# Performance work log

Hardware: AMD Instinct MI355X
Metric: run time of the kernel (lower is better)

The kernel has to match this reference:

```python
import jax, jax.numpy as jnp
import numpy as np

NEG = -1e30  # safe -inf surrogate (avoids nan grads through where)
NUM_CLASSES = 128
BLANK = NUM_CLASSES - 1
B, T, L = 256, 512, 64


def setup_inputs() -> dict:
    key = jax.random.key(0)
    k1, k2, k3, k4 = jax.random.split(key, 4)
    y_pred = jax.random.normal(k1, (B, T, NUM_CLASSES), dtype=jnp.float32)
    y_true = jax.random.randint(k2, (B, L), 0, BLANK, dtype=jnp.int32)  # labels in [0, C-2]
    input_length = jax.random.randint(k3, (B,), T // 2, T + 1, dtype=jnp.int32)
    label_length = jax.random.randint(k4, (B,), L // 2, L + 1, dtype=jnp.int32)
    return {"y_true": y_true, "y_pred": y_pred,
            "input_length": input_length, "label_length": label_length}


def ctc_loss(y_pred, y_true, input_length, label_length):
    # y_pred: [B,T,C] logits (batch-major), y_true: [B,L] int labels, blank = C-1.
    Bs, Ts, C = y_pred.shape
    Ls = y_true.shape[1]
    S = 2 * Ls + 1  # extended label lattice: blank, l1, blank, l2, ..., blank
    lp = jax.nn.log_softmax(y_pred.astype(jnp.float32), axis=-1)  # [B,T,C]
    z = jnp.full((Bs, S), BLANK, dtype=jnp.int32).at[:, 1::2].set(y_true)  # [B,S]
    idx = jnp.broadcast_to(z[:, None, :], (Bs, Ts, S))
    lp_z = jnp.take_along_axis(lp, idx, axis=2)  # [B,T,S] log p(z_s | t)
    # skip transition s-2 -> s allowed when z_s is a label differing from z_{s-2}
    s_idx = jnp.arange(S)
    z_m2 = jnp.pad(z[:, :-2], ((0, 0), (2, 0)), constant_values=BLANK)
    skip = (s_idx[None, :] >= 2) & (z != BLANK) & (z != z_m2)  # [B,S]
    alpha0 = (jnp.full((Bs, S), NEG, jnp.float32)
              .at[:, 0].set(lp_z[:, 0, 0])
              .at[:, 1].set(lp_z[:, 0, 1]))
    lps = jnp.moveaxis(lp_z[:, 1:, :], 1, 0)  # [T-1, B, S]
    ts = jnp.arange(1, Ts)

    def step(alpha, xs):
        t, lpt = xs
        a1 = jnp.pad(alpha[:, :-1], ((0, 0), (1, 0)), constant_values=NEG)
        a2 = jnp.where(skip, jnp.pad(alpha[:, :-2], ((0, 0), (2, 0)), constant_values=NEG), NEG)
        new = jnp.logaddexp(jnp.logaddexp(alpha, a1), a2) + lpt
        # freeze rows whose sequence already ended (t >= input_length)
        alpha = jnp.where((t < input_length)[:, None], new, alpha)
        return alpha, None

    alphaT, _ = jax.lax.scan(step, alpha0, (ts, lps))
    e1 = (2 * label_length)[:, None]  # final blank position per row
    a_end = jnp.take_along_axis(alphaT, e1, axis=1)[:, 0]
    a_end2 = jnp.take_along_axis(alphaT, e1 - 1, axis=1)[:, 0]
    return -jnp.logaddexp(a_end, a_end2)  # [B] negative log-likelihood


def reference(y_true, y_pred, input_length, label_length):
    # tf.nn.ctc_loss(labels, logits, label_length, logit_length,
    #                logits_time_major=False, blank_index=num_classes-1)
    return ctc_loss(y_pred, y_true, input_length, label_length)
```

## Files before the change

### kernel.cpp

```cpp
#include <hip/hip_runtime.h>
#include <hip/hip_fp16.h>
#include <math.h>


constexpr int Cc = 128;
constexpr int Tt = 512;
constexpr int Ll = 64;
constexpr float INV_LN2 = 1.4426950408889634f;
constexpr float LN2_F   = 0.6931471805599453f;

__device__ __forceinline__ float fexp2(float x) { return __builtin_amdgcn_exp2f(x); }
__device__ __forceinline__ float flog2(float x) { return __builtin_amdgcn_logf(x); }

template<int CTRL, bool BC>
__device__ __forceinline__ float dppf(float old, float x) {
    return __int_as_float(__builtin_amdgcn_update_dpp(
        __float_as_int(old), __float_as_int(x), CTRL, 0xF, 0xF, BC));
}
__device__ __forceinline__ float wshr1(float x, float fill) { return dppf<0x138, false>(fill, x); }

__device__ __forceinline__ float rlf(float v, int lane) {
    return __int_as_float(__builtin_amdgcn_readlane(__float_as_int(v), lane));
}

__device__ __forceinline__ float rowsum(float e) {
    e += dppf<0x111, true>(0.f, e);
    e += dppf<0x112, true>(0.f, e);
    e += dppf<0x114, true>(0.f, e);
    e += dppf<0x118, true>(0.f, e);
    return e;
}
__device__ __forceinline__ float rowmax(float m) {
    m = fmaxf(m, dppf<0x111, true>(0.f, m));
    m = fmaxf(m, dppf<0x112, true>(0.f, m));
    m = fmaxf(m, dppf<0x114, true>(0.f, m));
    m = fmaxf(m, dppf<0x118, true>(0.f, m));
    return m;
}
__device__ __forceinline__ float allsum(float e) {
    e = rowsum(e);
    return (rlf(e, 15) + rlf(e, 31)) + (rlf(e, 47) + rlf(e, 63));
}
__device__ __forceinline__ float allmax(float m) {
    m = rowmax(m);
    return fmaxf(fmaxf(rlf(m, 15), rlf(m, 31)), fmaxf(rlf(m, 47), rlf(m, 63)));
}

__device__ __forceinline__ float bperm_f(int srclane, float v) {
    return __int_as_float(__builtin_amdgcn_ds_bpermute(srclane << 2, __float_as_int(v)));
}
__device__ __forceinline__ float gather4(float4 v, int srclane, int csel) {
    const float gx = bperm_f(srclane, v.x), gy = bperm_f(srclane, v.y);
    const float gz = bperm_f(srclane, v.z), gw = bperm_f(srclane, v.w);
    const float lo = (csel & 1) ? gy : gx;
    const float hi = (csel & 1) ? gw : gz;
    return (csel & 2) ? hi : lo;
}

__global__ __launch_bounds__(256, 1) void ctc_fused_kernel(
    const int* __restrict__ y_true,
    const float* __restrict__ y_pred,
    const int* __restrict__ in_len,
    const int* __restrict__ lab_len,
    float* __restrict__ lpb_ws,
    float* __restrict__ out)
{
    __shared__ __half w_lds[Tt * 64];

    const int b   = blockIdx.x;
    const int tid = threadIdx.x;
    const int w   = tid >> 6;
    const int l   = tid & 63;

    const int lab = y_true[b * Ll + l] & 127;
    const float* rowbase = y_pred + (size_t)b * Tt * Cc;
    float* lpb = lpb_ws + b * Tt;

    const int half = l >> 5, li = l & 31;
    const int srcA = lab >> 2;
    const int csel = lab & 3;
    const int tbase = w * 128;

    float4 vb[4];
#pragma unroll
    for (int j = 0; j < 4; ++j)
        vb[j] = ((const float4*)(rowbase + (size_t)(tbase + 2 * j + half) * Cc))[li];

    for (int i = 0; i < 64; i += 4) {
#pragma unroll
        for (int j = 0; j < 4; ++j) {
            const float4 v = vb[j];
            const int nx = i + 4 + j;
            if (nx < 64)
                vb[j] = ((const float4*)(rowbase + (size_t)(tbase + 2 * nx + half) * Cc))[li];

            const int rA = tbase + 2 * (i + j);
            const int rB = rA + 1;

            float e = (fexp2(v.x * INV_LN2) + fexp2(v.y * INV_LN2))
                    + (fexp2(v.z * INV_LN2) + fexp2(v.w * INV_LN2));
            e = rowsum(e);
            const float sA = rlf(e, 15) + rlf(e, 31);
            const float sB = rlf(e, 47) + rlf(e, 63);
            const float lsA = flog2(sA), lsB = flog2(sB);

            const float blA = rlf(v.w, 31);
            const float blB = rlf(v.w, 63);

            if (l == 0) {
                lpb[rA] = fmaf(blA, INV_LN2, -lsA);
                lpb[rB] = fmaf(blB, INV_LN2, -lsB);
            }

            const float xA = gather4(v, srcA, csel);
            const float xB = gather4(v, srcA + 32, csel);
            const float wA = fminf(fmaxf(fexp2((xA - blA) * INV_LN2), 6.1e-5f), 8192.0f);
            const float wB = fminf(fmaxf(fexp2((xB - blB) * INV_LN2), 6.1e-5f), 8192.0f);
            w_lds[rA * 64 + l] = __float2half(wA);
            w_lds[rB * 64 + l] = __float2half(wB);
        }
    }

    __syncthreads();
    if (w != 0) return;

    const int inlen = in_len[b];
    const int LLv   = lab_len[b];

    const int labp  = __shfl_up(lab, 1, 64);
    const float skf = ((l >= 1) && (lab != labp)) ? 1.0f : 0.0f;

    float cb8[8];
#pragma unroll
    for (int j = 0; j < 8; ++j) cb8[j] = lpb[j * 64 + l];

    float aO = 0.0f, aE = 0.0f, r0 = 1.0f;
    float Rtot = 0.0f;

#define STEP(W) {                                                         \
        const float pE = wshr1(aE, r0);      \
        const float pO = wshr1(aO, 0.0f);                 \
        const float nO = (fmaf(skf, pO, pE) + aO) * (W);                  \
        aE += aO;                                                         \
        aO = nO; }

#define RENORM() {                                                        \
        const float M_ = allmax(fmaxf(fmaxf(aO, aE), r0));                \
        int R_ = (int)(__float_as_uint(M_) >> 23) - 127;                  \
        R_ = (R_ < 0) ? 0 : ((R_ > 126) ? 126 : R_);                      \
        const float sc = __uint_as_float((unsigned)(127 - R_) << 23);     \
        aO = fminf(aO * sc, 4.0f);                                        \
        aE = fminf(aE * sc, 4.0f);                                        \
        r0 = fminf(r0 * sc, 4.0f);                                        \
        Rtot += (float)R_; }

    __half hA[8], hB[8];
#pragma unroll
    for (int q = 0; q < 8; ++q) hA[q] = w_lds[q * 64 + l];

    const int nfull = inlen >> 3;
    for (int cb = 0; cb < nfull; ++cb) {
        const int nx = (cb + 1 < Tt / 8) ? cb + 1 : Tt / 8 - 1;
#pragma unroll
        for (int q = 0; q < 8; ++q) hB[q] = w_lds[(nx * 8 + q) * 64 + l];
#pragma unroll
        for (int j = 0; j < 8; ++j) STEP(__half2float(hA[j]));
        RENORM();
#pragma unroll
        for (int q = 0; q < 8; ++q) hA[q] = hB[q];
    }
    const int t0 = nfull << 3;
    if (t0 < inlen) {
#pragma unroll
        for (int j = 0; j < 8; ++j)
            if (t0 + j < inlen) STEP(__half2float(hA[j]));
    }
#undef STEP
#undef RENORM

    float s = 0.0f;
#pragma unroll
    for (int j = 0; j < 8; ++j) s += (j * 64 + l < inlen) ? cb8[j] : 0.0f;
    const float cum_b = allsum(s);

    const float aEr = __shfl(aE, LLv - 1, 64);
    const float aOr = __shfl(aO, LLv - 1, 64);
    if (l == 0)
        out[b] = -LN2_F * (flog2(fmaxf(aEr + aOr, 1e-37f)) + Rtot + cum_b);
}

extern "C" void kernel_launch(void* const* d_in, const int* in_sizes, int n_in,
                              void* d_out, int out_size, void* d_ws, size_t ws_size,
                              hipStream_t stream) {
    const int*   y_true  = (const int*)d_in[0];
    const float* y_pred  = (const float*)d_in[1];
    const int*   in_len  = (const int*)d_in[2];
    const int*   lab_len = (const int*)d_in[3];
    float*       out     = (float*)d_out;
    float*       lpb_ws  = (float*)d_ws;

    ctc_fused_kernel<<<256, 256, 0, stream>>>(y_true, y_pred, in_len, lab_len, lpb_ws, out);
}
```

Baseline: 128.9 us.

## Split CTC into prep and chain kernels with packed fp16 weights in global workspace

Splits the fused kernel into a prep kernel that computes log-softmax blank terms and fp16 emission weights and writes them to a global workspace, packed as eight timesteps per lane in a uint4. A separate one-wave-per-batch chain kernel then runs the recursion, reading 128-bit loads prefetched 64 timesteps ahead. The aim is to take the LDS staging and the 3-of-4-idle-wave recursion out of the prep block and to make the weight loads wide. In exchange it adds a second launch and a round trip of the weights through global memory. A fused fallback is kept for small workspaces, and weights for lanes past the label length are zeroed.

Result: slower. 143.3 us (+11.2%).

```diff
diff --git a/kernel.cpp b/kernel.cpp
--- a/kernel.cpp
+++ b/kernel.cpp
@@ -6,6 +6,7 @@
 constexpr int Cc = 128;
 constexpr int Tt = 512;
 constexpr int Ll = 64;
+constexpr int NC = Tt / 8;
 constexpr float INV_LN2 = 1.4426950408889634f;
 constexpr float LN2_F   = 0.6931471805599453f;
 
@@ -22,7 +23,6 @@
 __device__ __forceinline__ float rlf(float v, int lane) {
     return __int_as_float(__builtin_amdgcn_readlane(__float_as_int(v), lane));
 }
-
 __device__ __forceinline__ float rowsum(float e) {
     e += dppf<0x111, true>(0.f, e);
     e += dppf<0x112, true>(0.f, e);
@@ -45,7 +45,6 @@
     m = rowmax(m);
     return fmaxf(fmaxf(rlf(m, 15), rlf(m, 31)), fmaxf(rlf(m, 47), rlf(m, 63)));
 }
-
 __device__ __forceinline__ float bperm_f(int srclane, float v) {
     return __int_as_float(__builtin_amdgcn_ds_bpermute(srclane << 2, __float_as_int(v)));
 }
@@ -57,29 +56,27 @@
     return (csel & 2) ? hi : lo;
 }
 
-__global__ __launch_bounds__(256, 1) void ctc_fused_kernel(
-    const int* __restrict__ y_true,
-    const float* __restrict__ y_pred,
-    const int* __restrict__ in_len,
+__global__ __launch_bounds__(256, 1) void ctc_prep_kernel(
+    const int* __restrict__ y_true, const float* __restrict__ y_pred,
     const int* __restrict__ lab_len,
-    float* __restrict__ lpb_ws,
-    float* __restrict__ out)
+    float* __restrict__ lpb_ws, __half* __restrict__ w_ws)
 {
-    __shared__ __half w_lds[Tt * 64];
-
     const int b   = blockIdx.x;
     const int tid = threadIdx.x;
     const int w   = tid >> 6;
     const int l   = tid & 63;
 
+    int LLv = lab_len[b]; if (LLv < 1) LLv = 1; if (LLv > Ll) LLv = Ll;
     const int lab = y_true[b * Ll + l] & 127;
     const float* rowbase = y_pred + (size_t)b * Tt * Cc;
     float* lpb = lpb_ws + b * Tt;
+    __half* wbase = w_ws + ((size_t)b * NC) * 64 * 8;
 
     const int half = l >> 5, li = l & 31;
     const int srcA = lab >> 2;
     const int csel = lab & 3;
     const int tbase = w * 128;
+    const bool live = (l < LLv);
 
     float4 vb[4];
 #pragma unroll
@@ -87,6 +84,7 @@
         vb[j] = ((const float4*)(rowbase + (size_t)(tbase + 2 * j + half) * Cc))[li];
 
     for (int i = 0; i < 64; i += 4) {
+        unsigned pw[4];
 #pragma unroll
         for (int j = 0; j < 4; ++j) {
             const float4 v = vb[j];
@@ -103,80 +101,223 @@
             const float sA = rlf(e, 15) + rlf(e, 31);
             const float sB = rlf(e, 47) + rlf(e, 63);
             const float lsA = flog2(sA), lsB = flog2(sB);
-
             const float blA = rlf(v.w, 31);
             const float blB = rlf(v.w, 63);
 
-            if (l == 0) {
-                lpb[rA] = fmaf(blA, INV_LN2, -lsA);
-                lpb[rB] = fmaf(blB, INV_LN2, -lsB);
-            }
+            if (l == 0)
+                ((float2*)(lpb + rA))[0] =
+                    make_float2(fmaf(blA, INV_LN2, -lsA), fmaf(blB, INV_LN2, -lsB));
 
             const float xA = gather4(v, srcA, csel);
             const float xB = gather4(v, srcA + 32, csel);
-            const float wA = fminf(fmaxf(fexp2((xA - blA) * INV_LN2), 6.1e-5f), 8192.0f);
-            const float wB = fminf(fmaxf(fexp2((xB - blB) * INV_LN2), 6.1e-5f), 8192.0f);
-            w_lds[rA * 64 + l] = __float2half(wA);
-            w_lds[rB * 64 + l] = __float2half(wB);
+            float wA = fminf(fmaxf(fexp2((xA - blA) * INV_LN2), 6.1e-5f), 8192.0f);
+            float wB = fminf(fmaxf(fexp2((xB - blB) * INV_LN2), 6.1e-5f), 8192.0f);
+            wA = live ? wA : 0.0f;
+            wB = live ? wB : 0.0f;
+            pw[j] = (unsigned)__half_as_ushort(__float2half(wA))
+                  | ((unsigned)__half_as_ushort(__float2half(wB)) << 16);
+        }
+        const int chunk = (tbase + 2 * i) >> 3;
+        ((uint4*)(wbase + ((size_t)chunk * 64 + l) * 8))[0] =
+            make_uint4(pw[0], pw[1], pw[2], pw[3]);
+    }
+}
+
+template<bool GUARD>
+__device__ __forceinline__ void do_chunk(uint4 raw, int t0, int inlen, float skf,
+                                         float& aO, float& aE, float& r0, float& Rtot)
+{
+    float dv[8];
+    {
+        const __half2 h0 = *reinterpret_cast<const __half2*>(&raw.x);
+        const __half2 h1 = *reinterpret_cast<const __half2*>(&raw.y);
+        const __half2 h2 = *reinterpret_cast<const __half2*>(&raw.z);
+        const __half2 h3 = *reinterpret_cast<const __half2*>(&raw.w);
+        dv[0] = __low2float(h0); dv[1] = __high2float(h0);
+        dv[2] = __low2float(h1); dv[3] = __high2float(h1);
+        dv[4] = __low2float(h2); dv[5] = __high2float(h2);
+        dv[6] = __low2float(h3); dv[7] = __high2float(h3);
+    }
+#pragma unroll
+    for (int j = 0; j < 8; ++j) {
+        if (!GUARD || (t0 + j < inlen)) {
+            const float pE = wshr1(aE, r0);
+            const float pO = wshr1(aO, 0.0f);
+            const float nO = (fmaf(skf, pO, pE) + aO) * dv[j];
+            aE += aO;
+            aO = nO;
+        }
+    }
+    const float M_ = allmax(fmaxf(fmaxf(aO, aE), r0));
+    int R_ = (int)(__float_as_uint(M_) >> 23) - 127;
+    R_ = (R_ < 0) ? 0 : ((R_ > 126) ? 126 : R_);
+    const float sc = __uint_as_float((unsigned)(127 - R_) << 23);
+    aO = fminf(aO * sc, 4.0f);
+    aE = fminf(aE * sc, 4.0f);
+    r0 = fminf(r0 * sc, 4.0f);
+    Rtot += (float)R_;
+}
+
+__global__ __launch_bounds__(64, 1) void ctc_chain_kernel(
+    const int* __restrict__ y_true, const int* __restrict__ in_len,
+    const int* __restrict__ lab_len,
+    const float* __restrict__ lpb_ws, const __half* __restrict__ w_ws,
+    float* __restrict__ out)
+{
+    const int b = blockIdx.x;
+    const int l = threadIdx.x;
+
+    int inlen = in_len[b]; if (inlen < 1) inlen = 1; if (inlen > Tt) inlen = Tt;
+    int LLv   = lab_len[b]; if (LLv < 1) LLv = 1; if (LLv > Ll) LLv = Ll;
+
+    const int lab  = y_true[b * Ll + l] & 127;
+    const int labp = __shfl_up(lab, 1, 64);
+    const float skf = ((l >= 1) && (lab != labp)) ? 1.0f : 0.0f;
+
+    const float* lpb = lpb_ws + b * Tt;
+    const uint4* wp  = (const uint4*)w_ws + (size_t)b * NC * 64;
+
+    float cb8[8];
+#pragma unroll
+    for (int j = 0; j < 8; ++j) cb8[j] = lpb[j * 64 + l];
+
+#define LOADGRP(G, BUF) { _Pragma("unroll")                               \
+        for (int c = 0; c < 8; ++c) BUF[c] = wp[(size_t)(((G) * 8 + c) * 64 + l)]; }
+
+    float aO = 0.0f, aE = 0.0f, r0 = 1.0f, Rtot = 0.0f;
+
+    uint4 A[8], Bv[8];
+    LOADGRP(0, A);
+
+    for (int g = 0; ; ) {
+        const int base = g * 64;
+        const bool full = (base + 64 <= inlen);
+        const bool last = (base + 64 >= inlen);
+        if (!last) LOADGRP(g + 1, Bv);
+        if (full) {
+#pragma unroll
+            for (int c = 0; c < 8; ++c)
+                do_chunk<false>(A[c], base + 8 * c, inlen, skf, aO, aE, r0, Rtot);
+        } else {
+#pragma unroll
+            for (int c = 0; c < 8; ++c) {
+                const int t0 = base + 8 * c;
+                if (t0 < inlen)
+                    do_chunk<true>(A[c], t0, inlen, skf, aO, aE, r0, Rtot);
+            }
+        }
+        if (last) break;
+#pragma unroll
+        for (int c = 0; c < 8; ++c) A[c] = Bv[c];
+        ++g;
+    }
+#undef LOADGRP
+
+    float s = 0.0f;
+#pragma unroll
+    for (int j = 0; j < 8; ++j) s += (j * 64 + l < inlen) ? cb8[j] : 0.0f;
+    const float cum_b = allsum(s);
+
+    const float aEr = __shfl(aE, LLv - 1, 64);
+    const float aOr = __shfl(aO, LLv - 1, 64);
+    if (l == 0)
+        out[b] = -LN2_F * (flog2(fmaxf(aEr + aOr, 1e-37f)) + Rtot + cum_b);
+}
+
+__global__ __launch_bounds__(256, 1) void ctc_fused_kernel(
+    const int* __restrict__ y_true, const float* __restrict__ y_pred,
+    const int* __restrict__ in_len, const int* __restrict__ lab_len,
+    float* __restrict__ lpb_ws, float* __restrict__ out)
+{
+    __shared__ __half w_lds[Tt * 64];
+
+    const int b   = blockIdx.x;
+    const int tid = threadIdx.x;
+    const int w   = tid >> 6;
+    const int l   = tid & 63;
+
+    int LLv = lab_len[b]; if (LLv < 1) LLv = 1; if (LLv > Ll) LLv = Ll;
+    const int lab = y_true[b * Ll + l] & 127;
+    const float* rowbase = y_pred + (size_t)b * Tt * Cc;
+    float* lpb = lpb_ws + b * Tt;
+
+    const int half = l >> 5, li = l & 31;
+    const int srcA = lab >> 2, csel = lab & 3;
+    const int tbase = w * 128;
+    const bool live = (l < LLv);
+
+    float4 vb[4];
+#pragma unroll
+    for (int j = 0; j < 4; ++j)
+        vb[j] = ((const float4*)(rowbase + (size_t)(tbase + 2 * j + half) * Cc))[li];
+
+    for (int i = 0; i < 64; i += 4) {
+#pragma unroll
+        for (int j = 0; j < 4; ++j) {
+            const float4 v = vb[j];
+            const int nx = i + 4 + j;
+            if (nx < 64)
+                vb[j] = ((const float4*)(rowbase + (size_t)(tbase + 2 * nx + half) * Cc))[li];
+            const int rA = tbase + 2 * (i + j), rB = rA + 1;
+            float e = (fexp2(v.x * INV_LN2) + fexp2(v.y * INV_LN2))
+                    + (fexp2(v.z * INV_LN2) + fexp2(v.w * INV_LN2));
+            e = rowsum(e);
+            const float sA = rlf(e, 15) + rlf(e, 31);
+            const float sB = rlf(e, 47) + rlf(e, 63);
+            const float lsA = flog2(sA), lsB = flog2(sB);
+            const float blA = rlf(v.w, 31), blB = rlf(v.w, 63);
+            if (l == 0)
+                ((float2*)(lpb + rA))[0] =
+                    make_float2(fmaf(blA, INV_LN2, -lsA), fmaf(blB, INV_LN2, -lsB));
+            const float xA = gather4(v, srcA, csel);
+            const float xB = gather4(v, srcA + 32, csel);
+            float wA = fminf(fmaxf(fexp2((xA - blA) * INV_LN2), 6.1e-5f), 8192.0f);
+            float wB = fminf(fmaxf(fexp2((xB - blB) * INV_LN2), 6.1e-5f), 8192.0f);
+            w_lds[rA * 64 + l] = __float2half(live ? wA : 0.0f);
+            w_lds[rB * 64 + l] = __float2half(live ? wB : 0.0f);
         }
     }
 
     __syncthreads();
     if (w != 0) return;
 
-    const int inlen = in_len[b];
-    const int LLv   = lab_len[b];
-
-    const int labp  = __shfl_up(lab, 1, 64);
+    int inlen = in_len[b]; if (inlen < 1) inlen = 1; if (inlen > Tt) inlen = Tt;
+    const int labp = __shfl_up(lab, 1, 64);
     const float skf = ((l >= 1) && (lab != labp)) ? 1.0f : 0.0f;
 
     float cb8[8];
 #pragma unroll
     for (int j = 0; j < 8; ++j) cb8[j] = lpb[j * 64 + l];
 
-    float aO = 0.0f, aE = 0.0f, r0 = 1.0f;
-    float Rtot = 0.0f;
-
-#define STEP(W) {                                                         \
-        const float pE = wshr1(aE, r0);      \
-        const float pO = wshr1(aO, 0.0f);                 \
-        const float nO = (fmaf(skf, pO, pE) + aO) * (W);                  \
-        aE += aO;                                                         \
-        aO = nO; }
-
-#define RENORM() {                                                        \
-        const float M_ = allmax(fmaxf(fmaxf(aO, aE), r0));                \
-        int R_ = (int)(__float_as_uint(M_) >> 23) - 127;                  \
-        R_ = (R_ < 0) ? 0 : ((R_ > 126) ? 126 : R_);                      \
-        const float sc = __uint_as_float((unsigned)(127 - R_) << 23);     \
-        aO = fminf(aO * sc, 4.0f);                                        \
-        aE = fminf(aE * sc, 4.0f);                                        \
-        r0 = fminf(r0 * sc, 4.0f);                                        \
-        Rtot += (float)R_; }
-
-    __half hA[8], hB[8];
-#pragma unroll
-    for (int q = 0; q < 8; ++q) hA[q] = w_lds[q * 64 + l];
+    float aO = 0.0f, aE = 0.0f, r0 = 1.0f, Rtot = 0.0f;
 
     const int nfull = inlen >> 3;
     for (int cb = 0; cb < nfull; ++cb) {
-        const int nx = (cb + 1 < Tt / 8) ? cb + 1 : Tt / 8 - 1;
-#pragma unroll
-        for (int q = 0; q < 8; ++q) hB[q] = w_lds[(nx * 8 + q) * 64 + l];
-#pragma unroll
-        for (int j = 0; j < 8; ++j) STEP(__half2float(hA[j]));
-        RENORM();
-#pragma unroll
-        for (int q = 0; q < 8; ++q) hA[q] = hB[q];
+        uint4 raw;
+        raw.x = *(const unsigned*)&w_lds[(cb * 8 + 0) * 64 + l * 2 / 2];
+        unsigned p0 = ((unsigned)__half_as_ushort(w_lds[(cb * 8 + 0) * 64 + l]))
+                    | ((unsigned)__half_as_ushort(w_lds[(cb * 8 + 1) * 64 + l]) << 16);
+        unsigned p1 = ((unsigned)__half_as_ushort(w_lds[(cb * 8 + 2) * 64 + l]))
+                    | ((unsigned)__half_as_ushort(w_lds[(cb * 8 + 3) * 64 + l]) << 16);
+        unsigned p2 = ((unsigned)__half_as_ushort(w_lds[(cb * 8 + 4) * 64 + l]))
+                    | ((unsigned)__half_as_ushort(w_lds[(cb * 8 + 5) * 64 + l]) << 16);
+        unsigned p3 = ((unsigned)__half_as_ushort(w_lds[(cb * 8 + 6) * 64 + l]))
+                    | ((unsigned)__half_as_ushort(w_lds[(cb * 8 + 7) * 64 + l]) << 16);
+        raw = make_uint4(p0, p1, p2, p3);
+        do_chunk<false>(raw, cb * 8, inlen, skf, aO, aE, r0, Rtot);
     }
     const int t0 = nfull << 3;
     if (t0 < inlen) {
-#pragma unroll
-        for (int j = 0; j < 8; ++j)
-            if (t0 + j < inlen) STEP(__half2float(hA[j]));
-    }
-#undef STEP
-#undef RENORM
+        unsigned p[4] = {0, 0, 0, 0};
+#pragma unroll
+        for (int j = 0; j < 8; ++j) {
+            if (t0 + j < Tt) {
+                const unsigned hv = __half_as_ushort(w_lds[(t0 + j) * 64 + l]);
+                p[j >> 1] |= hv << ((j & 1) * 16);
+            }
+        }
+        do_chunk<true>(make_uint4(p[0], p[1], p[2], p[3]), t0, inlen, skf, aO, aE, r0, Rtot);
+    }
 
     float s = 0.0f;
 #pragma unroll
@@ -197,7 +338,16 @@
     const int*   in_len  = (const int*)d_in[2];
     const int*   lab_len = (const int*)d_in[3];
     float*       out     = (float*)d_out;
-    float*       lpb_ws  = (float*)d_ws;
-
-    ctc_fused_kernel<<<256, 256, 0, stream>>>(y_true, y_pred, in_len, lab_len, lpb_ws, out);
-}
+
+    const size_t lpb_bytes = (size_t)256 * Tt * sizeof(float);
+    const size_t w_bytes   = (size_t)256 * NC * 64 * 8 * sizeof(__half);
+    float*  lpb = (float*)d_ws;
+    __half* wws = (__half*)((char*)d_ws + lpb_bytes);
+
+    if (ws_size >= lpb_bytes + w_bytes) {
+        ctc_prep_kernel<<<256, 256, 0, stream>>>(y_true, y_pred, lab_len, lpb, wws);
+        ctc_chain_kernel<<<256, 64, 0, stream>>>(y_true, in_len, lab_len, lpb, wws, out);
+    } else {
+        ctc_fused_kernel<<<256, 256, 0, stream>>>(y_true, y_pred, in_len, lab_len, lpb, out);
+    }
+}
```

## Widen preprocessing to 16 waves, pack fp16 weights per lane, drop workspace

Applied to the files above, without the earlier changes.

The block grows from 4 to 16 waves, so the log-softmax and weight preprocessing phase is split over four times as many threads and each wave handles 32 timesteps. The blank log-prob sum is now reduced in registers and shared memory rather than written to a global workspace and read back. The LDS weight layout becomes [chunk][lane][8], so the recurrence wave fetches 8 timesteps with one 16-byte load, and the tail chunk is handled by a guarded template. Weights for labels past label_length are zeroed, and the serial recurrence is still done by a single wave.

New measurement: 117.4 us. 8.9% less time.

```diff
diff --git a/kernel.cpp b/kernel.cpp
--- a/kernel.cpp
+++ b/kernel.cpp
@@ -22,7 +22,6 @@
 __device__ __forceinline__ float rlf(float v, int lane) {
     return __int_as_float(__builtin_amdgcn_readlane(__float_as_int(v), lane));
 }
-
 __device__ __forceinline__ float rowsum(float e) {
     e += dppf<0x111, true>(0.f, e);
     e += dppf<0x112, true>(0.f, e);
@@ -37,15 +36,10 @@
     m = fmaxf(m, dppf<0x118, true>(0.f, m));
     return m;
 }
-__device__ __forceinline__ float allsum(float e) {
-    e = rowsum(e);
-    return (rlf(e, 15) + rlf(e, 31)) + (rlf(e, 47) + rlf(e, 63));
-}
 __device__ __forceinline__ float allmax(float m) {
     m = rowmax(m);
     return fmaxf(fmaxf(rlf(m, 15), rlf(m, 31)), fmaxf(rlf(m, 47), rlf(m, 63)));
 }
-
 __device__ __forceinline__ float bperm_f(int srclane, float v) {
     return __int_as_float(__builtin_amdgcn_ds_bpermute(srclane << 2, __float_as_int(v)));
 }
@@ -57,41 +51,81 @@
     return (csel & 2) ? hi : lo;
 }
 
-__global__ __launch_bounds__(256, 1) void ctc_fused_kernel(
+template<bool GUARD>
+__device__ __forceinline__ void do_chunk(uint4 raw, int t0, int inlen, float skf,
+                                         float& aO, float& aE, float& r0, float& Rtot)
+{
+    float dv[8];
+    {
+        const __half2 h0 = *reinterpret_cast<const __half2*>(&raw.x);
+        const __half2 h1 = *reinterpret_cast<const __half2*>(&raw.y);
+        const __half2 h2 = *reinterpret_cast<const __half2*>(&raw.z);
+        const __half2 h3 = *reinterpret_cast<const __half2*>(&raw.w);
+        dv[0] = __low2float(h0); dv[1] = __high2float(h0);
+        dv[2] = __low2float(h1); dv[3] = __high2float(h1);
+        dv[4] = __low2float(h2); dv[5] = __high2float(h2);
+        dv[6] = __low2float(h3); dv[7] = __high2float(h3);
+    }
+#pragma unroll
+    for (int j = 0; j < 8; ++j) {
+        if (!GUARD || (t0 + j < inlen)) {
+            const float pE = wshr1(aE, r0);
+            const float pO = wshr1(aO, 0.0f);
+            const float nO = (fmaf(skf, pO, pE) + aO) * dv[j];
+            aE += aO;
+            aO = nO;
+        }
+    }
+    const float M_ = allmax(fmaxf(fmaxf(aO, aE), r0));
+    int R_ = (int)(__float_as_uint(M_) >> 23) - 127;
+    R_ = (R_ < 0) ? 0 : ((R_ > 126) ? 126 : R_);
+    const float sc = __uint_as_float((unsigned)(127 - R_) << 23);
+    aO = fminf(aO * sc, 4.0f);
+    aE = fminf(aE * sc, 4.0f);
+    r0 = fminf(r0 * sc, 4.0f);
+    Rtot += (float)R_;
+}
+
+__global__ __launch_bounds__(1024, 1) void ctc_fused2_kernel(
     const int* __restrict__ y_true,
     const float* __restrict__ y_pred,
     const int* __restrict__ in_len,
     const int* __restrict__ lab_len,
-    float* __restrict__ lpb_ws,
     float* __restrict__ out)
 {
-    __shared__ __half w_lds[Tt * 64];
+    __shared__ __half w_lds[Tt / 8][64][8];
+    __shared__ float  ps[16];
 
     const int b   = blockIdx.x;
     const int tid = threadIdx.x;
     const int w   = tid >> 6;
     const int l   = tid & 63;
 
+    int inlen = in_len[b]; if (inlen < 1) inlen = 1; if (inlen > Tt) inlen = Tt;
+    int LLv   = lab_len[b]; if (LLv < 1) LLv = 1; if (LLv > Ll) LLv = Ll;
+
     const int lab = y_true[b * Ll + l] & 127;
     const float* rowbase = y_pred + (size_t)b * Tt * Cc;
-    float* lpb = lpb_ws + b * Tt;
 
     const int half = l >> 5, li = l & 31;
     const int srcA = lab >> 2;
     const int csel = lab & 3;
-    const int tbase = w * 128;
+    const int tbase = w * 32;
+    const bool live = (l < LLv);
 
     float4 vb[4];
 #pragma unroll
     for (int j = 0; j < 4; ++j)
         vb[j] = ((const float4*)(rowbase + (size_t)(tbase + 2 * j + half) * Cc))[li];
 
-    for (int i = 0; i < 64; i += 4) {
+    float acc = 0.0f;
+
+    for (int i = 0; i < 16; i += 4) {
 #pragma unroll
         for (int j = 0; j < 4; ++j) {
             const float4 v = vb[j];
             const int nx = i + 4 + j;
-            if (nx < 64)
+            if (nx < 16)
                 vb[j] = ((const float4*)(rowbase + (size_t)(tbase + 2 * nx + half) * Cc))[li];
 
             const int rA = tbase + 2 * (i + j);
@@ -103,85 +137,49 @@
             const float sA = rlf(e, 15) + rlf(e, 31);
             const float sB = rlf(e, 47) + rlf(e, 63);
             const float lsA = flog2(sA), lsB = flog2(sB);
-
             const float blA = rlf(v.w, 31);
             const float blB = rlf(v.w, 63);
 
-            if (l == 0) {
-                lpb[rA] = fmaf(blA, INV_LN2, -lsA);
-                lpb[rB] = fmaf(blB, INV_LN2, -lsB);
-            }
+            const float lpbA = fmaf(blA, INV_LN2, -lsA);
+            const float lpbB = fmaf(blB, INV_LN2, -lsB);
+            acc += ((rA < inlen) ? lpbA : 0.0f) + ((rB < inlen) ? lpbB : 0.0f);
 
             const float xA = gather4(v, srcA, csel);
             const float xB = gather4(v, srcA + 32, csel);
-            const float wA = fminf(fmaxf(fexp2((xA - blA) * INV_LN2), 6.1e-5f), 8192.0f);
-            const float wB = fminf(fmaxf(fexp2((xB - blB) * INV_LN2), 6.1e-5f), 8192.0f);
-            w_lds[rA * 64 + l] = __float2half(wA);
-            w_lds[rB * 64 + l] = __float2half(wB);
+            float wA = fminf(fmaxf(fexp2((xA - blA) * INV_LN2), 6.1e-5f), 8192.0f);
+            float wB = fminf(fmaxf(fexp2((xB - blB) * INV_LN2), 6.1e-5f), 8192.0f);
+            wA = live ? wA : 0.0f;
+            wB = live ? wB : 0.0f;
+            const unsigned packed =
+                  (unsigned)__half_as_ushort(__float2half(wA))
+                | ((unsigned)__half_as_ushort(__float2half(wB)) << 16);
+            *(unsigned*)&w_lds[rA >> 3][l][rA & 7] = packed;
         }
     }
+    if (l == 0) ps[w] = acc;
 
     __syncthreads();
     if (w != 0) return;
 
-    const int inlen = in_len[b];
-    const int LLv   = lab_len[b];
-
-    const int labp  = __shfl_up(lab, 1, 64);
+    const int labp = __shfl_up(lab, 1, 64);
     const float skf = ((l >= 1) && (lab != labp)) ? 1.0f : 0.0f;
 
-    float cb8[8];
-#pragma unroll
-    for (int j = 0; j < 8; ++j) cb8[j] = lpb[j * 64 + l];
-
-    float aO = 0.0f, aE = 0.0f, r0 = 1.0f;
-    float Rtot = 0.0f;
-
-#define STEP(W) {                                                         \
-        const float pE = wshr1(aE, r0);      \
-        const float pO = wshr1(aO, 0.0f);                 \
-        const float nO = (fmaf(skf, pO, pE) + aO) * (W);                  \
-        aE += aO;                                                         \
-        aO = nO; }
-
-#define RENORM() {                                                        \
-        const float M_ = allmax(fmaxf(fmaxf(aO, aE), r0));                \
-        int R_ = (int)(__float_as_uint(M_) >> 23) - 127;                  \
-        R_ = (R_ < 0) ? 0 : ((R_ > 126) ? 126 : R_);                      \
-        const float sc = __uint_as_float((unsigned)(127 - R_) << 23);     \
-        aO = fminf(aO * sc, 4.0f);                                        \
-        aE = fminf(aE * sc, 4.0f);                                        \
-        r0 = fminf(r0 * sc, 4.0f);                                        \
-        Rtot += (float)R_; }
-
-    __half hA[8], hB[8];
-#pragma unroll
-    for (int q = 0; q < 8; ++q) hA[q] = w_lds[q * 64 + l];
-
-    const int nfull = inlen >> 3;
-    for (int cb = 0; cb < nfull; ++cb) {
-        const int nx = (cb + 1 < Tt / 8) ? cb + 1 : Tt / 8 - 1;
-#pragma unroll
-        for (int q = 0; q < 8; ++q) hB[q] = w_lds[(nx * 8 + q) * 64 + l];
-#pragma unroll
-        for (int j = 0; j < 8; ++j) STEP(__half2float(hA[j]));
-        RENORM();
-#pragma unroll
-        for (int q = 0; q < 8; ++q) hA[q] = hB[q];
-    }
-    const int t0 = nfull << 3;
-    if (t0 < inlen) {
-#pragma unroll
-        for (int j = 0; j < 8; ++j)
-            if (t0 + j < inlen) STEP(__half2float(hA[j]));
-    }
-#undef STEP
-#undef RENORM
-
-    float s = 0.0f;
-#pragma unroll
-    for (int j = 0; j < 8; ++j) s += (j * 64 + l < inlen) ? cb8[j] : 0.0f;
-    const float cum_b = allsum(s);
+    float aO = 0.0f, aE = 0.0f, r0 = 1.0f, Rtot = 0.0f;
+
+    const int nchunks = (inlen + 7) >> 3;
+    uint4 A = *(const uint4*)&w_lds[0][l][0];
+    for (int c = 0; c < nchunks; ++c) {
+        const int nx = (c + 1 < Tt / 8) ? c + 1 : Tt / 8 - 1;
+        const uint4 Bv = *(const uint4*)&w_lds[nx][l][0];
+        const int t0 = c * 8;
+        if (t0 + 8 <= inlen) do_chunk<false>(A, t0, inlen, skf, aO, aE, r0, Rtot);
+        else                 do_chunk<true >(A, t0, inlen, skf, aO, aE, r0, Rtot);
+        A = Bv;
+    }
+
+    float cum_b = 0.0f;
+#pragma unroll
+    for (int q = 0; q < 16; ++q) cum_b += ps[q];
 
     const float aEr = __shfl(aE, LLv - 1, 64);
     const float aOr = __shfl(aO, LLv - 1, 64);
@@ -197,7 +195,7 @@
     const int*   in_len  = (const int*)d_in[2];
     const int*   lab_len = (const int*)d_in[3];
     float*       out     = (float*)d_out;
-    float*       lpb_ws  = (float*)d_ws;
-
-    ctc_fused_kernel<<<256, 256, 0, stream>>>(y_true, y_pred, in_len, lab_len, lpb_ws, out);
-}
+    (void)d_ws; (void)ws_size;
+
+    ctc_fused2_kernel<<<256, 1024, 0, stream>>>(y_true, y_pred, in_len, lab_len, out);
+}
```
